# Optimization experiments

Measured on AMD Instinct MI355X. Metric: run time of the kernel, lower is better.

The kernel has to match this reference:

```python
import jax, jax.numpy as jnp
import numpy as np

N_HEAD = 16
EPS = 1e-6

def setup_inputs() -> dict:
    key = jax.random.key(0)
    ks = jax.random.split(key, 5)
    B, S, D = 2, 2048, 1024
    scale = 0.02
    return {
        "hidden_states": jax.random.normal(ks[0], (B, S, D), dtype=jnp.float32),
        "w_q": jax.random.normal(ks[1], (D, D), dtype=jnp.float32) * scale,
        "w_k": jax.random.normal(ks[2], (D, D), dtype=jnp.float32) * scale,
        "w_v": jax.random.normal(ks[3], (D, D), dtype=jnp.float32) * scale,
        "w_o": jax.random.normal(ks[4], (D, D), dtype=jnp.float32) * scale,
        "qk_norm_factor": jnp.float32(1.0 / np.sqrt(D // N_HEAD)),
    }

def reference(hidden_states, w_q, w_k, w_v, w_o, qk_norm_factor):
    B, S, D = hidden_states.shape
    H = N_HEAD
    hd = D // H
    # projections (torch Linear without bias: x @ W^T)
    q = jnp.einsum('bsd,ed->bse', hidden_states, w_q).reshape(B, S, H, hd).transpose(0, 2, 1, 3)
    k = jnp.einsum('bsd,ed->bse', hidden_states, w_k).reshape(B, S, H, hd).transpose(0, 2, 1, 3)
    v = jnp.einsum('bsd,ed->bse', hidden_states, w_v).reshape(B, S, H, hd).transpose(0, 2, 1, 3)
    # hypersphere (QK) normalization
    q = q / (jnp.linalg.norm(q, axis=-1, keepdims=True) + EPS)
    k = k / (jnp.linalg.norm(k, axis=-1, keepdims=True) + EPS)
    # scores [B,H,S,S], learned scale
    scores = jnp.einsum('bhqd,bhkd->bhqk', q, k) * qk_norm_factor
    causal = jnp.tril(jnp.ones((S, S), dtype=bool))
    scores = jnp.where(causal[None, None], scores, jnp.float32(-jnp.inf))
    probs = jax.nn.softmax(scores, axis=-1)
    attn = jnp.einsum('bhqk,bhkd->bhqd', probs, v)
    attn = attn.transpose(0, 2, 1, 3).reshape(B, S, D)
    out = jnp.einsum('bsd,ed->bse', attn, w_o)
    return out
```

## Files before the change

### kernel.cpp

```cpp
#include <hip/hip_runtime.h>
#include <hip/hip_bf16.h>

typedef __attribute__((ext_vector_type(8))) short short8;
typedef __attribute__((ext_vector_type(4))) short short4v;
typedef __attribute__((ext_vector_type(4))) float floatx4;

union BF8 { short8 v; __hip_bfloat16 b[8]; };
union BF4U { ushort4 u; __hip_bfloat16 b[4]; };
union S4U { uint2 u; short4v v; };

__device__ __forceinline__ short8 load8(const __hip_bfloat16* p) {
    return *reinterpret_cast<const short8*>(p);
}
__device__ __forceinline__ short4v load4(const __hip_bfloat16* p) {
    return *reinterpret_cast<const short4v*>(p);
}

__device__ __forceinline__ void storeC(float* p, float v) { *p = v; }
__device__ __forceinline__ void storeC(__hip_bfloat16* p, float v) { *p = __float2bfloat16(v); }

__device__ __forceinline__ unsigned pack_bf16(float a, float b) {
    unsigned ua = __float_as_uint(a) + 0x8000u;
    unsigned ub = __float_as_uint(b) + 0x8000u;
    return __builtin_amdgcn_perm(ub, ua, 0x07060302u);
}

__device__ __forceinline__ float exp2_fast(float x) {
#if __has_builtin(__builtin_amdgcn_exp2f)
    return __builtin_amdgcn_exp2f(x);
#else
    return __expf(x * 0.6931471805599453f);
#endif
}

#if __has_builtin(__builtin_amdgcn_mfma_f32_16x16x16_bf16)
__device__ __forceinline__ floatx4 mfma16(short4v a, short4v b, floatx4 c) {
    return __builtin_amdgcn_mfma_f32_16x16x16_bf16(a, b, c, 0, 0, 0);
}
#elif __has_builtin(__builtin_amdgcn_mfma_f32_16x16x16bf16_1k)
__device__ __forceinline__ floatx4 mfma16(short4v a, short4v b, floatx4 c) {
    return __builtin_amdgcn_mfma_f32_16x16x16bf16_1k(a, b, c, 0, 0, 0);
}
#else
__device__ __forceinline__ floatx4 mfma16(short4v a, short4v b, floatx4 c) {
    asm volatile("v_mfma_f32_16x16x16_bf16 %0, %1, %2, %0"
                 : "+v"(c) : "v"(a), "v"(b));
    return c;
}
#endif

__device__ __forceinline__ void gload_lds16(const __hip_bfloat16* g, __hip_bfloat16* l) {
    __builtin_amdgcn_global_load_lds(
        (const __attribute__((address_space(1))) void*)g,
        (__attribute__((address_space(3))) void*)l, 16, 0, 0);
}

__global__ __launch_bounds__(256) void cast_all(const float* __restrict__ hs,
                                                const float* __restrict__ wq,
                                                const float* __restrict__ wk,
                                                const float* __restrict__ wv,
                                                const float* __restrict__ wo,
                                                __hip_bfloat16* __restrict__ Xb,
                                                __hip_bfloat16* __restrict__ Wb) {
    int i = blockIdx.x * 256 + threadIdx.x;
    const float* src;
    __hip_bfloat16* dst;
    if (blockIdx.y == 0) {
        src = hs; dst = Xb;
    } else {
        int m = i >> 18;
        src = (m == 0) ? wq : (m == 1) ? wk : (m == 2) ? wv : wo;
        src -= (size_t)m * 1048576;
        dst = Wb;
    }
    float4 v = reinterpret_cast<const float4*>(src)[i];
    BF4U u;
    u.b[0] = __float2bfloat16(v.x);
    u.b[1] = __float2bfloat16(v.y);
    u.b[2] = __float2bfloat16(v.z);
    u.b[3] = __float2bfloat16(v.w);
    reinterpret_cast<ushort4*>(dst)[i] = u.u;
}

template <typename OutT>
__global__ __launch_bounds__(256) void gemm_bt(const __hip_bfloat16* __restrict__ A,
                                               const __hip_bfloat16* __restrict__ B0,
                                               OutT* __restrict__ C0,
                                               int N, int Kd,
                                               size_t zsB, size_t zsC,
                                               int normz, const float* __restrict__ scale_p) {
    __shared__ __hip_bfloat16 lA[128 * 32];
    __shared__ __hip_bfloat16 lB[128 * 32];
    const __hip_bfloat16* B = B0 + zsB * blockIdx.z;
    OutT* C = C0 + zsC * blockIdx.z;
    const int t = threadIdx.x;
    const int m0 = blockIdx.x * 128, n0 = blockIdx.y * 128;
    const int w = t >> 6, l = t & 63;
    const int wr = (w >> 1) * 64, wc = (w & 1) * 64;
    const int lr = l & 15, lq = l >> 4;

    const floatx4 zero4 = {0.f, 0.f, 0.f, 0.f};
    floatx4 acc[4][4];
#pragma unroll
    for (int mt = 0; mt < 4; ++mt)
#pragma unroll
        for (int nt = 0; nt < 4; ++nt) acc[mt][nt] = zero4;

    for (int k0 = 0; k0 < Kd; k0 += 32) {
#pragma unroll
        for (int i = 0; i < 2; ++i) {
            int flat = t + i * 256;
            int row = flat >> 2, ch = flat & 3;
            gload_lds16(A + (size_t)(m0 + row) * Kd + k0 + ch * 8, lA + flat * 8);
            gload_lds16(B + (size_t)(n0 + row) * Kd + k0 + ch * 8, lB + flat * 8);
        }
        __syncthreads();
        short8 af[4], bfr[4];
#pragma unroll
        for (int mt = 0; mt < 4; ++mt)
            af[mt] = load8(lA + (wr + mt * 16 + lr) * 32 + lq * 8);
#pragma unroll
        for (int nt = 0; nt < 4; ++nt)
            bfr[nt] = load8(lB + (wc + nt * 16 + lr) * 32 + lq * 8);
#pragma unroll
        for (int mt = 0; mt < 4; ++mt)
#pragma unroll
            for (int nt = 0; nt < 4; ++nt)
                acc[mt][nt] = __builtin_amdgcn_mfma_f32_16x16x32_bf16(
                    af[mt], bfr[nt], acc[mt][nt], 0, 0, 0);
        __syncthreads();
    }

    if (normz && blockIdx.z < 2) {
        const float fac = (blockIdx.z == 0) ? (*scale_p * 1.44269504f) : 1.0f;
#pragma unroll
        for (int mt = 0; mt < 4; ++mt)
#pragma unroll
            for (int r = 0; r < 4; ++r) {
                float ss = 0.f;
#pragma unroll
                for (int nt = 0; nt < 4; ++nt) {
                    float v = acc[mt][nt][r];
                    ss += v * v;
                }
                ss += __shfl_xor(ss, 1, 64);
                ss += __shfl_xor(ss, 2, 64);
                ss += __shfl_xor(ss, 4, 64);
                ss += __shfl_xor(ss, 8, 64);
                float inv = fac / (sqrtf(ss) + 1e-6f);
#pragma unroll
                for (int nt = 0; nt < 4; ++nt) acc[mt][nt][r] *= inv;
            }
    }

#pragma unroll
    for (int mt = 0; mt < 4; ++mt)
#pragma unroll
        for (int nt = 0; nt < 4; ++nt)
#pragma unroll
            for (int r = 0; r < 4; ++r) {
                int row = m0 + wr + mt * 16 + lq * 4 + r;
                int col = n0 + wc + nt * 16 + lr;
                storeC(C + (size_t)row * N + col, acc[mt][nt][r]);
            }
}

__global__ __launch_bounds__(256) void transpose_v(const __hip_bfloat16* __restrict__ V,
                                                   __hip_bfloat16* __restrict__ Vt) {
    const int S = 2048, D = 1024;
    __shared__ __hip_bfloat16 tile[64][72];
    int t = threadIdx.x;
    int s0 = blockIdx.x * 64;
    int bh = blockIdx.y, b = bh >> 4, h = bh & 15;
    const __hip_bfloat16* src = V + ((size_t)b * S) * D + h * 64;
#pragma unroll
    for (int i = 0; i < 2; ++i) {
        int flat = t + i * 256;
        int sr = flat >> 3, ch = flat & 7;
        *reinterpret_cast<short8*>(&tile[sr][ch * 8]) =
            load8(src + (size_t)(s0 + sr) * D + ch * 8);
    }
    __syncthreads();
    __hip_bfloat16* dst = Vt + (size_t)bh * 64 * S;
#pragma unroll
    for (int i = 0; i < 2; ++i) {
        int flat = t + i * 256;
        int d = flat >> 3, sc = flat & 7;
        BF8 u;
#pragma unroll
        for (int j = 0; j < 8; ++j) u.b[j] = tile[sc * 8 + j][d];
        *reinterpret_cast<short8*>(dst + (size_t)d * S + s0 + sc * 8) = u.v;
    }
}

__global__ __launch_bounds__(256) void flash_attn(const __hip_bfloat16* __restrict__ Q,
                                                  const __hip_bfloat16* __restrict__ K,
                                                  const __hip_bfloat16* __restrict__ Vt,
                                                  __hip_bfloat16* __restrict__ O) {
    const int S = 2048, D = 1024;
    __shared__ __align__(16) char smem[20480];
    const int t = threadIdx.x;
    const int w = t >> 6, l = t & 63;
    const int lr = l & 15, lq = l >> 4;
    const int id = blockIdx.x;
    const int bh = (id & 7) * 4 + ((id >> 3) & 3);
    const int pr = id >> 5;
    const int b = bh >> 4, h = bh & 15;
    const __hip_bfloat16* Qb = Q + ((size_t)b * S) * D + h * 64;
    const __hip_bfloat16* Kb = K + ((size_t)b * S) * D + h * 64;
    const __hip_bfloat16* Vb = Vt + (size_t)bh * 64 * S;
    float* buf = reinterpret_cast<float*>(smem);

#pragma unroll 1
    for (int tile = 0; tile < 2; ++tile) {
        const int jq = (tile == 0) ? (31 - pr) : pr;
        const int q0 = jq * 64;

        short8 bq[4][2];
#pragma unroll
        for (int nt = 0; nt < 4; ++nt)
#pragma unroll
            for (int kt = 0; kt < 2; ++kt)
                bq[nt][kt] = load8(Qb + (size_t)(q0 + nt * 16 + lr) * D + kt * 32 + lq * 8);

        const floatx4 zero4 = {0.f, 0.f, 0.f, 0.f};
        floatx4 oacc[4][4];
        float lsum[4] = {0.f, 0.f, 0.f, 0.f};
#pragma unroll
        for (int mt = 0; mt < 4; ++mt)
#pragma unroll
            for (int nt = 0; nt < 4; ++nt) oacc[mt][nt] = zero4;

        const int klast = 2 * jq + 1;
        const int kmask = 2 * jq;

        if (w <= klast) {
#pragma unroll 1
            for (int ks = w; ks <= klast; ks += 4) {
                const int k0 = ks * 32;
                short8 bk[2][2];
#pragma unroll
                for (int mt = 0; mt < 2; ++mt)
#pragma unroll
                    for (int kt = 0; kt < 2; ++kt)
                        bk[mt][kt] = load8(Kb + (size_t)(k0 + mt * 16 + lr) * D + kt * 32 + lq * 8);
                floatx4 sacc[2][4];
#pragma unroll
                for (int mt = 0; mt < 2; ++mt)
#pragma unroll
                    for (int nt = 0; nt < 4; ++nt) sacc[mt][nt] = zero4;
#pragma unroll
                for (int mt = 0; mt < 2; ++mt)
#pragma unroll
                    for (int nt = 0; nt < 4; ++nt)
#pragma unroll
                        for (int kt = 0; kt < 2; ++kt)
                            sacc[mt][nt] = __builtin_amdgcn_mfma_f32_16x16x32_bf16(
                                bk[mt][kt], bq[nt][kt], sacc[mt][nt], 0, 0, 0);
                short4v bv[2][4];
#pragma unroll
                for (int mt = 0; mt < 2; ++mt)
#pragma unroll
                    for (int ntd = 0; ntd < 4; ++ntd)
                        bv[mt][ntd] = load4(Vb + (size_t)(ntd * 16 + lr) * S + k0 + mt * 16 + lq * 4);
                const bool domask = ks >= kmask;
                short4v ap[2][4];
#pragma unroll
                for (int mt = 0; mt < 2; ++mt)
#pragma unroll
                    for (int nt = 0; nt < 4; ++nt) {
                        float p0 = exp2_fast(sacc[mt][nt][0]);
                        float p1 = exp2_fast(sacc[mt][nt][1]);
                        float p2 = exp2_fast(sacc[mt][nt][2]);
                        float p3 = exp2_fast(sacc[mt][nt][3]);
                        if (domask) {
                            const int qg = q0 + nt * 16 + lr;
                            const int kb = k0 + mt * 16 + lq * 4;
                            p0 = (kb + 0 <= qg) ? p0 : 0.f;
                            p1 = (kb + 1 <= qg) ? p1 : 0.f;
                            p2 = (kb + 2 <= qg) ? p2 : 0.f;
                            p3 = (kb + 3 <= qg) ? p3 : 0.f;
                        }
                        lsum[nt] += (p0 + p1) + (p2 + p3);
                        S4U u;
                        u.u.x = pack_bf16(p0, p1);
                        u.u.y = pack_bf16(p2, p3);
                        ap[mt][nt] = u.v;
                    }
#pragma unroll
                for (int mt = 0; mt < 2; ++mt)
#pragma unroll
                    for (int ntq = 0; ntq < 4; ++ntq)
#pragma unroll
                        for (int ntd = 0; ntd < 4; ++ntd)
                            oacc[ntq][ntd] = mfma16(ap[mt][ntq], bv[mt][ntd], oacc[ntq][ntd]);
            }
        }

#pragma unroll
        for (int nt = 0; nt < 4; ++nt) {
            float s = lsum[nt];
            s += __shfl_xor(s, 16, 64);
            s += __shfl_xor(s, 32, 64);
            lsum[nt] = s;
        }

        const int row = t >> 2, c0 = (t & 3) * 4;
        __hip_bfloat16* Ob = O + ((size_t)b * S) * D + h * 64;
        float inv = 0.f;
        __syncthreads();
#pragma unroll
        for (int chunk = 0; chunk < 4; ++chunk) {
#pragma unroll
            for (int mtq = 0; mtq < 4; ++mtq)
#pragma unroll
                for (int r = 0; r < 4; ++r)
                    buf[w * 1280 + (mtq * 16 + lq * 4 + r) * 20 + lr] = oacc[mtq][chunk][r];
            if (chunk == 0 && lq == 0) {
#pragma unroll
                for (int nt = 0; nt < 4; ++nt)
                    buf[w * 1280 + (nt * 16 + lr) * 20 + 16] = lsum[nt];
            }
            __syncthreads();
            if (chunk == 0) {
                float Lt = buf[row * 20 + 16] + buf[1280 + row * 20 + 16] +
                           buf[2560 + row * 20 + 16] + buf[3840 + row * 20 + 16];
                inv = 1.f / Lt;
            }
            float4 a = {0.f, 0.f, 0.f, 0.f};
#pragma unroll
            for (int w2 = 0; w2 < 4; ++w2) {
                float4 v = *reinterpret_cast<const float4*>(buf + w2 * 1280 + row * 20 + c0);
                a.x += v.x; a.y += v.y; a.z += v.z; a.w += v.w;
            }
            uint2 d;
            d.x = pack_bf16(a.x * inv, a.y * inv);
            d.y = pack_bf16(a.z * inv, a.w * inv);
            *reinterpret_cast<uint2*>(Ob + (size_t)(q0 + row) * D + chunk * 16 + c0) = d;
            if (chunk < 3) __syncthreads();
        }
    }
}

extern "C" void kernel_launch(void* const* d_in, const int* in_sizes, int n_in,
                              void* d_out, int out_size, void* d_ws, size_t ws_size,
                              hipStream_t stream) {
    const float* hs  = (const float*)d_in[0];
    const float* wq  = (const float*)d_in[1];
    const float* wk  = (const float*)d_in[2];
    const float* wv  = (const float*)d_in[3];
    const float* wo  = (const float*)d_in[4];
    const float* qkf = (const float*)d_in[5];

    char* ws = (char*)d_ws;
    const size_t MB = 1024 * 1024;
    __hip_bfloat16* Xb  = (__hip_bfloat16*)(ws);
    __hip_bfloat16* Wqb = (__hip_bfloat16*)(ws + 8 * MB);
    __hip_bfloat16* Wob = (__hip_bfloat16*)(ws + 14 * MB);
    __hip_bfloat16* Qb  = (__hip_bfloat16*)(ws + 16 * MB);
    __hip_bfloat16* Kb  = (__hip_bfloat16*)(ws + 24 * MB);
    __hip_bfloat16* Vb  = (__hip_bfloat16*)(ws + 32 * MB);
    __hip_bfloat16* Vt  = (__hip_bfloat16*)(ws + 40 * MB);
    __hip_bfloat16* Ab  = (__hip_bfloat16*)(ws + 48 * MB);

    cast_all<<<dim3(4096, 2), 256, 0, stream>>>(hs, wq, wk, wv, wo, Xb, Wqb);

    gemm_bt<__hip_bfloat16><<<dim3(32, 8, 3), 256, 0, stream>>>(
        Xb, Wqb, Qb, 1024, 1024, (size_t)1048576, (size_t)4194304, 1, qkf);

    transpose_v<<<dim3(32, 32), 256, 0, stream>>>(Vb, Vt);
    flash_attn<<<512, 256, 0, stream>>>(Qb, Kb, Vt, Ab);

    gemm_bt<float><<<dim3(32, 8, 1), 256, 0, stream>>>(
        Ab, Wob, (float*)d_out, 1024, 1024, (size_t)0, (size_t)0, 0, qkf);
}
```

Measured before the change: 204.8 us.

## Double-buffer K/V tiles per wave through LDS with async global-to-LDS loads

Each wave now prefetches its next K and V tiles straight into a private, XOR-swizzled LDS double buffer using global-to-LDS loads. It then reads its MFMA operands from LDS instead of issuing direct global loads inside the loop. The aim is to hide global memory latency behind the QK and PV MFMA work. In exchange, shared memory grows to 64KB per block and launch bounds are set to 2 blocks per CU, which limits occupancy.

```diff
diff --git a/kernel.cpp b/kernel.cpp
--- a/kernel.cpp
+++ b/kernel.cpp
@@ -193,12 +193,12 @@
     }
 }
 
-__global__ __launch_bounds__(256) void flash_attn(const __hip_bfloat16* __restrict__ Q,
-                                                  const __hip_bfloat16* __restrict__ K,
-                                                  const __hip_bfloat16* __restrict__ Vt,
-                                                  __hip_bfloat16* __restrict__ O) {
+__global__ __launch_bounds__(256, 2) void flash_attn(const __hip_bfloat16* __restrict__ Q,
+                                                     const __hip_bfloat16* __restrict__ K,
+                                                     const __hip_bfloat16* __restrict__ Vt,
+                                                     __hip_bfloat16* __restrict__ O) {
     const int S = 2048, D = 1024;
-    __shared__ __align__(16) char smem[20480];
+    __shared__ __align__(16) char smem[65536];
     const int t = threadIdx.x;
     const int w = t >> 6, l = t & 63;
     const int lr = l & 15, lq = l >> 4;
@@ -209,7 +209,11 @@
     const __hip_bfloat16* Qb = Q + ((size_t)b * S) * D + h * 64;
     const __hip_bfloat16* Kb = K + ((size_t)b * S) * D + h * 64;
     const __hip_bfloat16* Vb = Vt + (size_t)bh * 64 * S;
+    __hip_bfloat16* wbase = reinterpret_cast<__hip_bfloat16*>(smem) + w * 8192;
     float* buf = reinterpret_cast<float*>(smem);
+
+    const int kr = l >> 3, ksg = (l & 7) ^ (kr & 7);
+    const int vr = l >> 2, vsg = (l & 3) ^ (vr & 3);
 
 #pragma unroll 1
     for (int tile = 0; tile < 2; ++tile) {
@@ -235,15 +239,54 @@
         const int kmask = 2 * jq;
 
         if (w <= klast) {
+            {
+                const int k0 = w * 32;
+#pragma unroll
+                for (int i = 0; i < 4; ++i)
+                    gload_lds16(Kb + (size_t)(k0 + i * 8 + kr) * D + ksg * 8,
+                                wbase + i * 512 + l * 8);
+#pragma unroll
+                for (int i = 0; i < 4; ++i)
+                    gload_lds16(Vb + (size_t)(i * 16 + vr) * S + k0 + vsg * 8,
+                                wbase + 4096 + i * 512 + l * 8);
+            }
+            int p = 0;
 #pragma unroll 1
             for (int ks = w; ks <= klast; ks += 4) {
                 const int k0 = ks * 32;
+                asm volatile("s_waitcnt vmcnt(0)" ::: "memory");
+                const __hip_bfloat16* kb = wbase + p * 2048;
+                const __hip_bfloat16* vb = wbase + 4096 + p * 2048;
                 short8 bk[2][2];
 #pragma unroll
                 for (int mt = 0; mt < 2; ++mt)
 #pragma unroll
-                    for (int kt = 0; kt < 2; ++kt)
-                        bk[mt][kt] = load8(Kb + (size_t)(k0 + mt * 16 + lr) * D + kt * 32 + lq * 8);
+                    for (int kt = 0; kt < 2; ++kt) {
+                        const int rl = mt * 16 + lr;
+                        const int sg = (kt * 4 + lq) ^ (rl & 7);
+                        bk[mt][kt] = load8(kb + rl * 64 + sg * 8);
+                    }
+                short4v bv[2][4];
+#pragma unroll
+                for (int mt = 0; mt < 2; ++mt)
+#pragma unroll
+                    for (int ntd = 0; ntd < 4; ++ntd) {
+                        const int rl = ntd * 16 + lr;
+                        const int sg = (mt * 2 + (lq >> 1)) ^ (rl & 3);
+                        bv[mt][ntd] = load4(vb + rl * 32 + sg * 8 + (lq & 1) * 4);
+                    }
+                if (ks + 4 <= klast) {
+                    const int kn = (ks + 4) * 32;
+                    __hip_bfloat16* nb = wbase + (p ^ 1) * 2048;
+#pragma unroll
+                    for (int i = 0; i < 4; ++i)
+                        gload_lds16(Kb + (size_t)(kn + i * 8 + kr) * D + ksg * 8,
+                                    nb + i * 512 + l * 8);
+#pragma unroll
+                    for (int i = 0; i < 4; ++i)
+                        gload_lds16(Vb + (size_t)(i * 16 + vr) * S + kn + vsg * 8,
+                                    nb + 4096 + i * 512 + l * 8);
+                }
                 floatx4 sacc[2][4];
 #pragma unroll
                 for (int mt = 0; mt < 2; ++mt)
@@ -257,12 +300,6 @@
                         for (int kt = 0; kt < 2; ++kt)
                             sacc[mt][nt] = __builtin_amdgcn_mfma_f32_16x16x32_bf16(
                                 bk[mt][kt], bq[nt][kt], sacc[mt][nt], 0, 0, 0);
-                short4v bv[2][4];
-#pragma unroll
-                for (int mt = 0; mt < 2; ++mt)
-#pragma unroll
-                    for (int ntd = 0; ntd < 4; ++ntd)
-                        bv[mt][ntd] = load4(Vb + (size_t)(ntd * 16 + lr) * S + k0 + mt * 16 + lq * 4);
                 const bool domask = ks >= kmask;
                 short4v ap[2][4];
 #pragma unroll
@@ -275,11 +312,11 @@
                         float p3 = exp2_fast(sacc[mt][nt][3]);
                         if (domask) {
                             const int qg = q0 + nt * 16 + lr;
-                            const int kb = k0 + mt * 16 + lq * 4;
-                            p0 = (kb + 0 <= qg) ? p0 : 0.f;
-                            p1 = (kb + 1 <= qg) ? p1 : 0.f;
-                            p2 = (kb + 2 <= qg) ? p2 : 0.f;
-                            p3 = (kb + 3 <= qg) ? p3 : 0.f;
+                            const int kb2 = k0 + mt * 16 + lq * 4;
+                            p0 = (kb2 + 0 <= qg) ? p0 : 0.f;
+                            p1 = (kb2 + 1 <= qg) ? p1 : 0.f;
+                            p2 = (kb2 + 2 <= qg) ? p2 : 0.f;
+                            p3 = (kb2 + 3 <= qg) ? p3 : 0.f;
                         }
                         lsum[nt] += (p0 + p1) + (p2 + p3);
                         S4U u;
@@ -294,6 +331,7 @@
 #pragma unroll
                         for (int ntd = 0; ntd < 4; ++ntd)
                             oacc[ntq][ntd] = mfma16(ap[mt][ntq], bv[mt][ntd], oacc[ntq][ntd]);
+                p ^= 1;
             }
         }
 
```

New measurement: 184.6 us. 1.11x faster.
